# Performance work log

Measured on AMD Instinct MI355X. Metric: run time of the kernel, lower is better.

## Reference

```python
import jax, jax.numpy as jnp
import numpy as np

N_ATOMS = 100          # n_atoms from init_kwargs
BATCH = 1024           # dataset / batch size (single-batch usage per docstring)


def setup_inputs() -> dict:
    key = jax.random.key(0)
    k1, k2 = jax.random.split(key)
    # descriptors = pairwise distances between atoms -> 6 nonzero derivs per desc per frame
    ii, jj = np.triu_indices(N_ATOMS, 1)               # [D] each
    D = ii.shape[0]                                    # 4950 descriptors
    atoms = np.stack([ii, jj], axis=1)                 # [D, 2]
    atom_pd = np.repeat(atoms, 3, axis=1).reshape(-1)  # [D*6]: i,i,i,j,j,j per desc
    dim_pd = np.tile(np.array([0, 1, 2, 0, 1, 2]), D)  # [D*6]
    des_pd = np.repeat(np.arange(D), 6)                # [D*6]

    batch_ind = np.repeat(np.arange(BATCH), D * 6)     # [nnz]
    des_ind = np.tile(des_pd, BATCH)                   # [nnz]
    atom_ind = np.tile(atom_pd, BATCH)                 # [nnz]
    dim_ind = np.tile(dim_pd, BATCH)                   # [nnz]
    # faithful shifted index: per-frame offset + atom*3 + dim
    scatter_idx = batch_ind * (N_ATOMS * 3) + atom_ind * 3 + dim_ind

    nnz = batch_ind.shape[0]
    x = jax.random.normal(k1, (BATCH, D), dtype=jnp.float32)      # dq/d(descriptors)
    left = jax.random.normal(k2, (nnz,), dtype=jnp.float32)       # nonzero d(desc)/d(pos)
    return {
        "x": x,
        "left": left,
        "batch_ind": jnp.asarray(batch_ind, jnp.int32),
        "des_ind": jnp.asarray(des_ind, jnp.int32),
        "scatter_idx": jnp.asarray(scatter_idx, jnp.int32),
    }


def reference(x, left, batch_ind, des_ind, scatter_idx):
    # gather right operand: dq/d(desc) for each nonzero left entry
    right = x[batch_ind, des_ind]                      # [nnz]
    src = left * right                                 # chain rule terms
    # scatter-add into (frame, atom, dim) bins, then square (square modulus comps)
    acc = jax.ops.segment_sum(src, scatter_idx, num_segments=BATCH * N_ATOMS * 3)
    return (acc * acc).reshape(BATCH, N_ATOMS * 3)
```

## Files before the change

kernel.cpp:

```cpp
#include <hip/hip_runtime.h>


#define D_DESC  4950
#define BATCH   1024
#define NOUT    300
#define NWAVES  8

__device__ __forceinline__ int rowstart(int i) { return (i * (199 - i)) >> 1; }

__global__ __launch_bounds__(512, 8)
void sd_kernel(const float* __restrict__ x,
               const float* __restrict__ left,
               float* __restrict__ out)
{
    __shared__ __align__(16) float acc[NOUT];

    const int b    = blockIdx.x;
    const int tid  = threadIdx.x;
    const int lane = tid & 63;
    const int w    = tid >> 6;

    if (tid < NOUT) acc[tid] = 0.0f;
    __syncthreads();

    const float* __restrict__ Lb = left + (size_t)b * (D_DESC * 6);
    const float* __restrict__ xb = x    + (size_t)b * D_DESC;

    for (int i = w; i < 99; i += NWAVES) {
        const int rs  = rowstart(i);
        const int len = 99 - i;
        const int nf  = len * 6;
        const int n2  = nf >> 1;
        const float2* __restrict__ base2 = (const float2*)(Lb + rs * 6);
        const float*  __restrict__ xrow  = xb + rs;
        const int jb3 = (i + 1) * 3;

        float s0 = 0.f, s1 = 0.f, s2 = 0.f;

        int dl = (lane << 2) / 6;
        int r  = (lane << 2) - 6 * dl;
        int p2 = lane << 1;

        const int niter = (n2 + 127) >> 7;
        for (int m = 0; m < niter; ++m) {
            if (p2 < n2) {
                const float2 L = base2[p2];
                const float xv = xrow[dl];
                const float za = L.x * xv;
                const float zb = L.y * xv;
                if (r == 0) {
                    s0 += za; s1 += zb;
                } else if (r == 2) {
                    s2 += za;
                    atomicAdd(&acc[jb3 + dl * 3 + 0], zb);
                } else {
                    atomicAdd(&acc[jb3 + dl * 3 + 1], za);
                    atomicAdd(&acc[jb3 + dl * 3 + 2], zb);
                }
            }
            if (p2 + 1 < n2) {
                const int dB = (r == 4) ? dl + 1 : dl;
                const int rB = (r == 4) ? 0 : r + 2;
                const float2 L = base2[p2 + 1];
                const float xv = xrow[dB];
                const float za = L.x * xv;
                const float zb = L.y * xv;
                if (rB == 0) {
                    s0 += za; s1 += zb;
                } else if (rB == 2) {
                    s2 += za;
                    atomicAdd(&acc[jb3 + dB * 3 + 0], zb);
                } else {
                    atomicAdd(&acc[jb3 + dB * 3 + 1], za);
                    atomicAdd(&acc[jb3 + dB * 3 + 2], zb);
                }
            }
            dl += (r >= 2) ? 43 : 42;
            r   = (r >= 2) ? r - 2 : r + 4;
            p2 += 128;
        }

        const int nact = (nf + 3) >> 2;
        #pragma unroll
        for (int off = 32; off >= 1; off >>= 1) {
            if (nact > off) {
                s0 += __shfl_down(s0, off);
                s1 += __shfl_down(s1, off);
                s2 += __shfl_down(s2, off);
            }
        }
        if (lane == 0) {
            atomicAdd(&acc[i * 3 + 0], s0);
            atomicAdd(&acc[i * 3 + 1], s1);
            atomicAdd(&acc[i * 3 + 2], s2);
        }
    }
    __syncthreads();

    if (tid < NOUT / 4) {
        const float4 v = ((const float4*)acc)[tid];
        float4 o;
        o.x = v.x * v.x; o.y = v.y * v.y;
        o.z = v.z * v.z; o.w = v.w * v.w;
        ((float4*)(out + (size_t)b * NOUT))[tid] = o;
    }
}

extern "C" void kernel_launch(void* const* d_in, const int* in_sizes, int n_in,
                              void* d_out, int out_size, void* d_ws, size_t ws_size,
                              hipStream_t stream) {
    (void)in_sizes; (void)n_in; (void)d_ws; (void)ws_size; (void)out_size;
    const float* x    = (const float*)d_in[0];
    const float* left = (const float*)d_in[1];
    sd_kernel<<<BATCH, 512, 0, stream>>>(x, left, (float*)d_out);
}
```

Measured before the change: 391.1 us.

## Replace shared-memory atomics with per-wave private accumulators and descriptor-per-lane mapping

Each lane now handles one descriptor (six contiguous left values) instead of interleaved float2 pairs, which removes the remainder/branch bookkeeping. Column contributions go into per-wave private float4 slots in LDS using plain read-modify-write, and row sums go into a separate row array, so no atomics are needed. A final pass sums the eight wave copies per atom. This trades atomic contention and branch divergence for more LDS use, strided 24-byte loads per lane that coalesce less well, and a serial final reduction across waves.

Measured after the change: 339.4 us. -13.2%, faster.

```diff
diff --git a/kernel.cpp b/kernel.cpp
--- a/kernel.cpp
+++ b/kernel.cpp
@@ -1,10 +1,10 @@
 #include <hip/hip_runtime.h>
 
 
-#define D_DESC  4950
-#define BATCH   1024
-#define NOUT    300
-#define NWAVES  8
+#define D_DESC 4950
+#define BATCH  1024
+#define NOUT   300
+#define NW     8
 
 __device__ __forceinline__ int rowstart(int i) { return (i * (199 - i)) >> 1; }
 
@@ -13,74 +13,47 @@
                const float* __restrict__ left,
                float* __restrict__ out)
 {
-    __shared__ __align__(16) float acc[NOUT];
+    __shared__ float4 cacc[NW * 100];
+    __shared__ float4 racc[100];
 
     const int b    = blockIdx.x;
     const int tid  = threadIdx.x;
     const int lane = tid & 63;
     const int w    = tid >> 6;
 
-    if (tid < NOUT) acc[tid] = 0.0f;
-    __syncthreads();
+    for (int t = lane; t < 100; t += 64)
+        cacc[w * 100 + t] = float4{0.f, 0.f, 0.f, 0.f};
+    if (tid == 0) racc[99] = float4{0.f, 0.f, 0.f, 0.f};
 
     const float* __restrict__ Lb = left + (size_t)b * (D_DESC * 6);
     const float* __restrict__ xb = x    + (size_t)b * D_DESC;
 
-    for (int i = w; i < 99; i += NWAVES) {
-        const int rs  = rowstart(i);
-        const int len = 99 - i;
-        const int nf  = len * 6;
-        const int n2  = nf >> 1;
-        const float2* __restrict__ base2 = (const float2*)(Lb + rs * 6);
-        const float*  __restrict__ xrow  = xb + rs;
-        const int jb3 = (i + 1) * 3;
-
+    for (int a = w; a < 99; a += NW) {
+        const int len = 99 - a;
+        const int rs  = rowstart(a);
+        const float* __restrict__ base = Lb + rs * 6;
         float s0 = 0.f, s1 = 0.f, s2 = 0.f;
 
-        int dl = (lane << 2) / 6;
-        int r  = (lane << 2) - 6 * dl;
-        int p2 = lane << 1;
-
-        const int niter = (n2 + 127) >> 7;
-        for (int m = 0; m < niter; ++m) {
-            if (p2 < n2) {
-                const float2 L = base2[p2];
-                const float xv = xrow[dl];
-                const float za = L.x * xv;
-                const float zb = L.y * xv;
-                if (r == 0) {
-                    s0 += za; s1 += zb;
-                } else if (r == 2) {
-                    s2 += za;
-                    atomicAdd(&acc[jb3 + dl * 3 + 0], zb);
-                } else {
-                    atomicAdd(&acc[jb3 + dl * 3 + 1], za);
-                    atomicAdd(&acc[jb3 + dl * 3 + 2], zb);
-                }
+        for (int d0 = 0; d0 < len; d0 += 64) {
+            const int d = d0 + lane;
+            if (d < len) {
+                const float2 c01 = *(const float2*)(base + d * 6);
+                const float2 c23 = *(const float2*)(base + d * 6 + 2);
+                const float2 c45 = *(const float2*)(base + d * 6 + 4);
+                const float xv = xb[rs + d];
+                s0 += c01.x * xv;
+                s1 += c01.y * xv;
+                s2 += c23.x * xv;
+                float4* slot = &cacc[w * 100 + (a + 1 + d)];
+                float4 cur = *slot;
+                cur.x += c23.y * xv;
+                cur.y += c45.x * xv;
+                cur.z += c45.y * xv;
+                *slot = cur;
             }
-            if (p2 + 1 < n2) {
-                const int dB = (r == 4) ? dl + 1 : dl;
-                const int rB = (r == 4) ? 0 : r + 2;
-                const float2 L = base2[p2 + 1];
-                const float xv = xrow[dB];
-                const float za = L.x * xv;
-                const float zb = L.y * xv;
-                if (rB == 0) {
-                    s0 += za; s1 += zb;
-                } else if (rB == 2) {
-                    s2 += za;
-                    atomicAdd(&acc[jb3 + dB * 3 + 0], zb);
-                } else {
-                    atomicAdd(&acc[jb3 + dB * 3 + 1], za);
-                    atomicAdd(&acc[jb3 + dB * 3 + 2], zb);
-                }
-            }
-            dl += (r >= 2) ? 43 : 42;
-            r   = (r >= 2) ? r - 2 : r + 4;
-            p2 += 128;
         }
 
-        const int nact = (nf + 3) >> 2;
+        const int nact = len < 64 ? len : 64;
         #pragma unroll
         for (int off = 32; off >= 1; off >>= 1) {
             if (nact > off) {
@@ -89,20 +62,21 @@
                 s2 += __shfl_down(s2, off);
             }
         }
-        if (lane == 0) {
-            atomicAdd(&acc[i * 3 + 0], s0);
-            atomicAdd(&acc[i * 3 + 1], s1);
-            atomicAdd(&acc[i * 3 + 2], s2);
-        }
+        if (lane == 0) racc[a] = float4{s0, s1, s2, 0.f};
     }
     __syncthreads();
 
-    if (tid < NOUT / 4) {
-        const float4 v = ((const float4*)acc)[tid];
-        float4 o;
-        o.x = v.x * v.x; o.y = v.y * v.y;
-        o.z = v.z * v.z; o.w = v.w * v.w;
-        ((float4*)(out + (size_t)b * NOUT))[tid] = o;
+    if (tid < 100) {
+        float4 v = racc[tid];
+        #pragma unroll
+        for (int ww = 0; ww < NW; ++ww) {
+            const float4 c = cacc[ww * 100 + tid];
+            v.x += c.x; v.y += c.y; v.z += c.z;
+        }
+        float* __restrict__ o = out + (size_t)b * NOUT + tid * 3;
+        o[0] = v.x * v.x;
+        o[1] = v.y * v.y;
+        o[2] = v.z * v.z;
     }
 }
 
```
